# Kernel optimization log

Measured on AMD Instinct MI355X. Metric: run time of the kernel, lower is better.

The kernel has to match this reference:

```python
import jax, jax.numpy as jnp
import numpy as np

DS = 32   # self_obs_dim
DO = 32   # obstacle_obs_dim
D = DS + DO
H = 128   # obstacle_hidden_size
B = 512   # batch_size
A = 16    # num_adv_obs = 2 * num_oppo_obs


def _init_linear(key, fan_in, fan_out):
    kw, kb = jax.random.split(key)
    bound = 1.0 / np.sqrt(fan_in)
    w = jax.random.uniform(kw, (fan_in, fan_out), jnp.float32, -bound, bound)
    b = jax.random.uniform(kb, (fan_out,), jnp.float32, -bound, bound)
    return w, b


def setup_inputs() -> dict:
    key = jax.random.key(0)
    ks = jax.random.split(key, 10)
    obs = jax.random.normal(ks[0], (B, DS), jnp.float32)
    latent = jax.random.normal(ks[1], (B, A, DO), jnp.float32)
    hw1, hb1 = _init_linear(ks[2], D, H)
    hw2, hb2 = _init_linear(ks[3], H, D * H)
    vw1, vb1 = _init_linear(ks[4], H, H)
    vw2, vb2 = _init_linear(ks[5], H, H)
    aw1, ab1 = _init_linear(ks[6], 2 * H, H)
    aw2, ab2 = _init_linear(ks[7], H, H)
    aw3, ab3 = _init_linear(ks[8], H, 1)
    return {
        "obs": obs, "obs_intention_latent": latent,
        "hw1": hw1, "hb1": hb1, "hw2": hw2, "hb2": hb2,
        "vw1": vw1, "vb1": vb1, "vw2": vw2, "vb2": vb2,
        "aw1": aw1, "ab1": ab1, "aw2": aw2, "ab2": ab2,
        "aw3": aw3, "ab3": ab3,
        "num_adv_obs": A, "batch_size": B, "num_groups": 1,
    }


def reference(obs, obs_intention_latent, hw1, hb1, hw2, hb2,
              vw1, vb1, vw2, vb2, aw1, ab1, aw2, ab2, aw3, ab3,
              num_adv_obs, batch_size, num_groups):
    relu = jax.nn.relu
    # flatten opponents (batch-major, matches torch .reshape)
    obs_obstacles = obs_intention_latent.reshape(-1, DO)          # [N, DO]
    # torch .repeat(num_adv_obs, 1) tiles the batch dim
    self_rep = jnp.tile(obs[:, :DS], (num_adv_obs, 1))            # [N, DS]
    mlp_input = jnp.concatenate([self_rep, obs_obstacles], axis=1)  # [N, D]
    # hypernet: per-sample weight [N, D, H]
    h = relu(mlp_input @ hw1 + hb1)
    w = relu(h @ hw2 + hb2).reshape(-1, D, H)
    # per-sample vector-matrix product + tanh
    emb = jnp.tanh(jnp.einsum("nd,ndh->nh", mlp_input, w))        # [N, H]
    # neighbor value MLP
    vals = relu(relu(emb @ vw1 + vb1) @ vw2 + vb2)                # [N, H]
    # attention: concat with per-batch mean embedding
    emb_mean = jnp.mean(emb.reshape(batch_size, -1, H), axis=1)   # [B, H]
    mean_rep = jnp.tile(emb_mean, (num_adv_obs, 1))               # [N, H]
    att_in = jnp.concatenate([emb, mean_rep], axis=1)             # [N, 2H]
    scores = relu(relu(att_in @ aw1 + ab1) @ aw2 + ab2) @ aw3 + ab3  # [N, 1]
    att = jax.nn.softmax(scores.reshape(batch_size, -1), axis=1).reshape(-1, 1)
    weighted = (att * vals).reshape(batch_size, -1, H)
    return jnp.sum(weighted, axis=1)                              # [B, H]
```

## Files before the change

kernel.cpp:

```cpp
#include <hip/hip_runtime.h>
#include <hip/hip_bf16.h>
#include <math.h>

#define BATCH 512
#define NADV  16
#define NROWS (BATCH*NADV)
#define DS    32
#define DO    32
#define DIM   64
#define HID   128
#define WCOLS (DIM*HID)
#define LSTR  136
#define PACK_BLOCKS 276

typedef _Float16 half8 __attribute__((ext_vector_type(8)));
typedef float floatx4 __attribute__((ext_vector_type(4)));

#define XSW(c) ((((c) >> 2) & 7) << 2)

__global__ __launch_bounds__(256)
void k_prep(const float* __restrict__ obs, const float* __restrict__ latent,
            const float* __restrict__ hw1, const float* __restrict__ hb1,
            const float* __restrict__ hw2, const float* __restrict__ vw1,
            const float* __restrict__ vw2, const float* __restrict__ aw1,
            const float* __restrict__ aw2,
            _Float16* __restrict__ hf,
            _Float16* __restrict__ w2p, _Float16* __restrict__ vw1p,
            _Float16* __restrict__ vw2p, _Float16* __restrict__ aw1p,
            _Float16* __restrict__ aw2p) {
    __shared__ __align__(16) float smem[32 * 132];
    int b = blockIdx.x;
    int tid = threadIdx.x;
    if (b < PACK_BLOCKS) {
        const float* src; _Float16* dst; int N, Kt, jb, kt;
        if (b < 256)      { src = hw2; dst = w2p;  N = WCOLS; Kt = 4; jb = b >> 2; kt = b & 3; }
        else if (b < 260) { src = vw1; dst = vw1p; N = HID;   Kt = 4; jb = 0; kt = b - 256; }
        else if (b < 264) { src = vw2; dst = vw2p; N = HID;   Kt = 4; jb = 0; kt = b - 260; }
        else if (b < 272) { src = aw1; dst = aw1p; N = HID;   Kt = 8; jb = 0; kt = b - 264; }
        else              { src = aw2; dst = aw2p; N = HID;   Kt = 4; jb = 0; kt = b - 272; }
        for (int i = tid; i < 32 * 32; i += 256) {
            int r = i >> 5, c4 = (i & 31) * 4;
            *(float4*)&smem[r * 132 + c4] =
                *(const float4*)(src + (size_t)(kt * 32 + r) * N + jb * 128 + c4);
        }
        __syncthreads();
        for (int i = tid; i < 8 * 64; i += 256) {
            int ctl = i >> 6, ln = i & 63;
            int ct = jb * 8 + ctl;
            int rbase = (ln >> 4) * 8, cc = ctl * 16 + (ln & 15);
            half8 v;
#pragma unroll
            for (int e = 0; e < 8; ++e) v[e] = (_Float16)smem[(rbase + e) * 132 + cc];
            *(half8*)(dst + ((size_t)ct * Kt + kt) * 512 + ln * 8) = v;
        }
    } else {
        int n0 = (b - PACK_BLOCKS) * 16;
        int wave = tid >> 6, lane = tid & 63, l15 = lane & 15, quad = lane >> 4;
        half8 af2[2];
        {
            int n = n0 + l15;
            const float* orow = obs + (size_t)(n & (BATCH - 1)) * DS + quad * 8;
            const float* lrow = latent + (size_t)n * DO + quad * 8;
#pragma unroll
            for (int e = 0; e < 8; ++e) {
                af2[0][e] = (_Float16)orow[e];
                af2[1][e] = (_Float16)lrow[e];
            }
        }
#pragma unroll
        for (int cti = 0; cti < 2; ++cti) {
            int ct = wave * 2 + cti;
            float bb = hb1[ct * 16 + l15];
            floatx4 acc = {bb, bb, bb, bb};
#pragma unroll
            for (int ks = 0; ks < 2; ++ks) {
                const float* wsrc = hw1 + (size_t)(ks * 32 + quad * 8) * HID + ct * 16 + l15;
                half8 bf;
#pragma unroll
                for (int e = 0; e < 8; ++e) bf[e] = (_Float16)wsrc[(size_t)e * HID];
                acc = __builtin_amdgcn_mfma_f32_16x16x32_f16(af2[ks], bf, acc, 0, 0, 0);
            }
#pragma unroll
            for (int reg = 0; reg < 4; ++reg)
                hf[(size_t)(n0 + quad * 4 + reg) * HID + ct * 16 + l15] =
                    (_Float16)fmaxf(acc[reg], 0.f);
        }
    }
}

__global__ __launch_bounds__(256, 2)
void k_gemm(const _Float16* __restrict__ hf, const _Float16* __restrict__ w2p,
            const float* __restrict__ hb2, const float* __restrict__ obs,
            const float* __restrict__ latent,
            _Float16* __restrict__ embf, _Float16* __restrict__ emeanf) {
    __shared__ __align__(16) char smraw[16384 + 128];
    float (*xs_t)[64] = (float(*)[64])smraw;

    int b   = blockIdx.x;
    int tid = threadIdx.x;
    int wave = tid >> 6, lane = tid & 63, l15 = lane & 15, quad = lane >> 4;

    int jt = b & 7;
    int rt = b >> 3;
    int n0 = rt * 64;
    int j0 = jt * 16;

    for (int i = tid; i < 64 * 16; i += 256) {
        int r = i >> 4, c4 = (i & 15) * 4;
        float4 v;
        if (c4 < DS) v = *(const float4*)(obs + ((n0 + r) & (BATCH - 1)) * DS + c4);
        else         v = *(const float4*)(latent + (size_t)(n0 + r) * DO + (c4 - DS));
        xs_t[c4 + 0][r ^ XSW(c4 + 0)] = v.x;
        xs_t[c4 + 1][r ^ XSW(c4 + 1)] = v.y;
        xs_t[c4 + 2][r ^ XSW(c4 + 2)] = v.z;
        xs_t[c4 + 3][r ^ XSW(c4 + 3)] = v.w;
    }

    half8 af[4][4];
#pragma unroll
    for (int t = 0; t < 4; ++t)
#pragma unroll
        for (int ks = 0; ks < 4; ++ks)
            af[t][ks] = *(const half8*)(hf + (size_t)(n0 + t * 16 + l15) * HID
                                           + ks * 32 + quad * 8);
    __syncthreads();

    float emb_acc[4][4];
#pragma unroll
    for (int t = 0; t < 4; ++t)
#pragma unroll
        for (int reg = 0; reg < 4; ++reg) emb_acc[t][reg] = 0.f;

    const _Float16* wbase = w2p + (size_t)jt * 2048 + lane * 8;
    const _Float16* wp = wbase + (size_t)(wave * 16) * 16384;
    half8 b0 = *(const half8*)(wp + 0 * 512);
    half8 b1 = *(const half8*)(wp + 1 * 512);
    half8 b2 = *(const half8*)(wp + 2 * 512);
    half8 b3 = *(const half8*)(wp + 3 * 512);

#pragma unroll 2
    for (int i = 0; i < 16; ++i) {
        int d = wave * 16 + i;
        half8 n0_, n1_, n2_, n3_;
        if (i < 15) {
            const _Float16* np = wbase + (size_t)(d + 1) * 16384;
            n0_ = *(const half8*)(np + 0 * 512);
            n1_ = *(const half8*)(np + 1 * 512);
            n2_ = *(const half8*)(np + 2 * 512);
            n3_ = *(const half8*)(np + 3 * 512);
        }
        float bb = hb2[d * HID + j0 + l15];
        int rsw = XSW(d);
#pragma unroll
        for (int t = 0; t < 4; ++t) {
            floatx4 acc = {bb, bb, bb, bb};
            acc = __builtin_amdgcn_mfma_f32_16x16x32_f16(af[t][0], b0, acc, 0, 0, 0);
            acc = __builtin_amdgcn_mfma_f32_16x16x32_f16(af[t][1], b1, acc, 0, 0, 0);
            acc = __builtin_amdgcn_mfma_f32_16x16x32_f16(af[t][2], b2, acc, 0, 0, 0);
            acc = __builtin_amdgcn_mfma_f32_16x16x32_f16(af[t][3], b3, acc, 0, 0, 0);
            floatx4 xv = *(const floatx4*)&xs_t[d][(t * 16 + quad * 4) ^ rsw];
#pragma unroll
            for (int reg = 0; reg < 4; ++reg)
                emb_acc[t][reg] = fmaf(xv[reg], fmaxf(acc[reg], 0.f), emb_acc[t][reg]);
        }
        b0 = n0_; b1 = n1_; b2 = n2_; b3 = n3_;
    }
    __syncthreads();

    float* red = (float*)smraw;
#pragma unroll
    for (int t = 0; t < 4; ++t)
#pragma unroll
        for (int reg = 0; reg < 4; ++reg)
            red[(wave * 64 + t * 16 + quad * 4 + reg) * 16 + l15] = emb_acc[t][reg];
    __syncthreads();

    {
        float e[4];
#pragma unroll
        for (int rr = 0; rr < 4; ++rr) {
            int row = wave * 16 + quad * 4 + rr;
            float s = red[(0 * 64 + row) * 16 + l15] + red[(1 * 64 + row) * 16 + l15]
                    + red[(2 * 64 + row) * 16 + l15] + red[(3 * 64 + row) * 16 + l15];
            e[rr] = tanhf(s);
            embf[(size_t)(n0 + row) * HID + j0 + l15] = (_Float16)e[rr];
        }
        float m = e[0] + e[1] + e[2] + e[3];
        m += __shfl_xor(m, 16, 64);
        m += __shfl_xor(m, 32, 64);
        if (quad == 0)
            emeanf[(size_t)(rt * 4 + wave) * HID + j0 + l15] =
                (_Float16)(m * (1.f / 16));
    }
}

__global__ __launch_bounds__(512, 4)
void k_tail(const _Float16* __restrict__ embf, const _Float16* __restrict__ emeanf,
            const _Float16* __restrict__ vw1p, const float* __restrict__ vb1,
            const _Float16* __restrict__ vw2p, const float* __restrict__ vb2,
            const _Float16* __restrict__ aw1p, const float* __restrict__ ab1,
            const _Float16* __restrict__ aw2p, const float* __restrict__ ab2,
            const float* __restrict__ aw3, const float* __restrict__ ab3,
            float* __restrict__ out) {
    __shared__ _Float16 embs[16][LSTR];
    __shared__ _Float16 means[16][LSTR];
    __shared__ _Float16 tAs[16][LSTR];
    __shared__ _Float16 tBs[16][LSTR];
    __shared__ float scr[16][32];
    __shared__ float satt[16];
    __shared__ float att[16];
    int g = blockIdx.x;
    int n0 = g * 16;
    int tid = threadIdx.x;
    int wave = tid >> 6, lane = tid & 63, l15 = lane & 15, quad = lane >> 4;
    int ct = wave;

    {
        int m = tid >> 8, r = (tid >> 4) & 15, c8 = (tid & 15) * 8;
        if (m == 0)
            *(half8*)&embs[r][c8] = *(const half8*)(embf + (size_t)(n0 + r) * HID + c8);
        else
            *(half8*)&means[r][c8] =
                *(const half8*)(emeanf + (size_t)((n0 & 511) + r) * HID + c8);
    }
    __syncthreads();

    half8 av[4], amean[4];
#pragma unroll
    for (int ks = 0; ks < 4; ++ks) {
        av[ks]    = *(const half8*)&embs[l15][ks * 32 + quad * 8];
        amean[ks] = *(const half8*)&means[l15][ks * 32 + quad * 8];
    }

    floatx4 acc;
    {
        float bb = vb1[ct * 16 + l15];
        acc = (floatx4){bb, bb, bb, bb};
    }
#pragma unroll
    for (int ks = 0; ks < 4; ++ks) {
        half8 bfr = *(const half8*)(vw1p + ((size_t)ct * 4 + ks) * 512 + lane * 8);
        acc = __builtin_amdgcn_mfma_f32_16x16x32_f16(av[ks], bfr, acc, 0, 0, 0);
    }
#pragma unroll
    for (int reg = 0; reg < 4; ++reg)
        tAs[quad * 4 + reg][ct * 16 + l15] = (_Float16)fmaxf(acc[reg], 0.f);
    __syncthreads();

    half8 at[4];
#pragma unroll
    for (int ks = 0; ks < 4; ++ks)
        at[ks] = *(const half8*)&tAs[l15][ks * 32 + quad * 8];

    floatx4 vacc;
    {
        float bb = vb2[ct * 16 + l15];
        vacc = (floatx4){bb, bb, bb, bb};
    }
#pragma unroll
    for (int ks = 0; ks < 4; ++ks) {
        half8 bfr = *(const half8*)(vw2p + ((size_t)ct * 4 + ks) * 512 + lane * 8);
        vacc = __builtin_amdgcn_mfma_f32_16x16x32_f16(at[ks], bfr, vacc, 0, 0, 0);
    }

    floatx4 aacc;
    {
        float bb = ab1[ct * 16 + l15];
        aacc = (floatx4){bb, bb, bb, bb};
    }
#pragma unroll
    for (int ks = 0; ks < 8; ++ks) {
        half8 bfr = *(const half8*)(aw1p + ((size_t)ct * 8 + ks) * 512 + lane * 8);
        half8 a = (ks < 4) ? av[ks] : amean[ks - 4];
        aacc = __builtin_amdgcn_mfma_f32_16x16x32_f16(a, bfr, aacc, 0, 0, 0);
    }
#pragma unroll
    for (int reg = 0; reg < 4; ++reg)
        tBs[quad * 4 + reg][ct * 16 + l15] = (_Float16)fmaxf(aacc[reg], 0.f);
    __syncthreads();

    half8 aa[4];
#pragma unroll
    for (int ks = 0; ks < 4; ++ks)
        aa[ks] = *(const half8*)&tBs[l15][ks * 32 + quad * 8];

    floatx4 a2acc;
    {
        float bb = ab2[ct * 16 + l15];
        a2acc = (floatx4){bb, bb, bb, bb};
    }
#pragma unroll
    for (int ks = 0; ks < 4; ++ks) {
        half8 bfr = *(const half8*)(aw2p + ((size_t)ct * 4 + ks) * 512 + lane * 8);
        a2acc = __builtin_amdgcn_mfma_f32_16x16x32_f16(aa[ks], bfr, a2acc, 0, 0, 0);
    }
    __syncthreads();
#pragma unroll
    for (int reg = 0; reg < 4; ++reg)
        tAs[quad * 4 + reg][ct * 16 + l15] = (_Float16)fmaxf(a2acc[reg], 0.f);
    __syncthreads();

    {
        int r = tid >> 5, ch = tid & 31;
        float p = 0.f;
#pragma unroll
        for (int k = 0; k < 4; ++k)
            p += (float)tAs[r][ch * 4 + k] * aw3[ch * 4 + k];
        scr[r][ch] = p;
    }
    __syncthreads();
    if (tid < 16) {
        float s = ab3[0];
#pragma unroll
        for (int ch = 0; ch < 32; ++ch) s += scr[tid][ch];
        satt[tid] = s;
    }
    __syncthreads();
    if (tid < 16) {
        float m = -1e30f;
#pragma unroll
        for (int a = 0; a < 16; ++a) m = fmaxf(m, satt[a]);
        float S = 0.f;
#pragma unroll
        for (int a = 0; a < 16; ++a) S += expf(satt[a] - m);
        att[tid] = expf(satt[tid] - m) / S;
    }
    __syncthreads();

    {
        float p = 0.f;
#pragma unroll
        for (int reg = 0; reg < 4; ++reg)
            p += att[quad * 4 + reg] * fmaxf(vacc[reg], 0.f);
        p += __shfl_xor(p, 16, 64);
        p += __shfl_xor(p, 32, 64);
        if (quad == 0) out[(size_t)g * HID + ct * 16 + l15] = p;
    }
}

extern "C" void kernel_launch(void* const* d_in, const int* in_sizes, int n_in,
                              void* d_out, int out_size, void* d_ws, size_t ws_size,
                              hipStream_t stream) {
    const float* obs = (const float*)d_in[0];
    const float* lat = (const float*)d_in[1];
    const float* hw1 = (const float*)d_in[2];
    const float* hb1 = (const float*)d_in[3];
    const float* hw2 = (const float*)d_in[4];
    const float* hb2 = (const float*)d_in[5];
    const float* vw1 = (const float*)d_in[6];
    const float* vb1 = (const float*)d_in[7];
    const float* vw2 = (const float*)d_in[8];
    const float* vb2 = (const float*)d_in[9];
    const float* aw1 = (const float*)d_in[10];
    const float* ab1 = (const float*)d_in[11];
    const float* aw2 = (const float*)d_in[12];
    const float* ab2 = (const float*)d_in[13];
    const float* aw3 = (const float*)d_in[14];
    const float* ab3 = (const float*)d_in[15];
    float* out = (float*)d_out;

    char* ws = (char*)d_ws;
    _Float16*  hf     = (_Float16*)ws;  ws += (size_t)NROWS * HID * 2;
    _Float16*  w2p    = (_Float16*)ws;  ws += (size_t)WCOLS * HID * 2;
    _Float16*  embf   = (_Float16*)ws;  ws += (size_t)NROWS * HID * 2;
    _Float16*  emeanf = (_Float16*)ws;  ws += (size_t)BATCH * HID * 2;
    _Float16*  vw1p   = (_Float16*)ws;  ws += (size_t)HID * HID * 2;
    _Float16*  vw2p   = (_Float16*)ws;  ws += (size_t)HID * HID * 2;
    _Float16*  aw1p   = (_Float16*)ws;  ws += (size_t)2 * HID * HID * 2;
    _Float16*  aw2p   = (_Float16*)ws;  ws += (size_t)HID * HID * 2;

    hipLaunchKernelGGL(k_prep, dim3(PACK_BLOCKS + NROWS / 16), dim3(256), 0, stream,
                       obs, lat, hw1, hb1, hw2, vw1, vw2, aw1, aw2,
                       hf, w2p, vw1p, vw2p, aw1p, aw2p);
    hipLaunchKernelGGL(k_gemm, dim3(1024), dim3(256), 0, stream,
                       hf, w2p, hb2, obs, lat, embf, emeanf);
    hipLaunchKernelGGL(k_tail, dim3(BATCH), dim3(512), 0, stream,
                       embf, emeanf, vw1p, vb1, vw2p, vb2,
                       aw1p, ab1, aw2p, ab2, aw3, ab3, out);
}
```

Baseline: 134.5 us.

## Stream hypernet weight tiles into LDS with async double-buffered global_load_lds

The main hypernet GEMM kernel now stages each wave's weight tiles into a per-wave double-buffered LDS region using global_load_lds, prefetching two d-steps ahead with explicit vmcnt waits. Before, it used register prefetch of the next step. The bias slice is also preloaded into shared memory instead of being read from global memory on every iteration. The aim is to hide global-load latency better and lower register pressure so occupancy can go to 3 blocks per CU. In exchange, LDS use grows to about 52KB per block, and correctness depends on hand-placed waitcnt counts and scheduling barriers.

Result: no change. 132.6 us (-1.4%).

```diff
diff --git a/kernel.cpp b/kernel.cpp
--- a/kernel.cpp
+++ b/kernel.cpp
@@ -15,6 +15,12 @@
 
 typedef _Float16 half8 __attribute__((ext_vector_type(8)));
 typedef float floatx4 __attribute__((ext_vector_type(4)));
+
+__device__ inline void async_ld16(void* lds, const void* g) {
+    __builtin_amdgcn_global_load_lds(
+        (const __attribute__((address_space(1))) void*)g,
+        (__attribute__((address_space(3))) void*)lds, 16, 0, 0);
+}
 
 #define XSW(c) ((((c) >> 2) & 7) << 2)
 
@@ -88,13 +94,15 @@
     }
 }
 
-__global__ __launch_bounds__(256, 2)
-void k_gemm(const _Float16* __restrict__ hf, const _Float16* __restrict__ w2p,
-            const float* __restrict__ hb2, const float* __restrict__ obs,
-            const float* __restrict__ latent,
-            _Float16* __restrict__ embf, _Float16* __restrict__ emeanf) {
-    __shared__ __align__(16) char smraw[16384 + 128];
-    float (*xs_t)[64] = (float(*)[64])smraw;
+__global__ __launch_bounds__(256, 3)
+void k_hyper(const _Float16* __restrict__ hf, const _Float16* __restrict__ w2p,
+             const float* __restrict__ hb2, const float* __restrict__ obs,
+             const float* __restrict__ latent,
+             _Float16* __restrict__ embf, _Float16* __restrict__ emeanf) {
+    __shared__ __align__(16) char smraw[53248];
+    _Float16 (*Bs)[2][2048] = (_Float16(*)[2][2048])smraw;
+    float (*xs_t)[64] = (float(*)[64])(smraw + 32768);
+    float* bias_s = (float*)(smraw + 49152);
 
     int b   = blockIdx.x;
     int tid = threadIdx.x;
@@ -115,6 +123,8 @@
         xs_t[c4 + 2][r ^ XSW(c4 + 2)] = v.z;
         xs_t[c4 + 3][r ^ XSW(c4 + 3)] = v.w;
     }
+    for (int i = tid; i < 64 * 16; i += 256)
+        bias_s[i] = hb2[(i >> 4) * HID + j0 + (i & 15)];
 
     half8 af[4][4];
 #pragma unroll
@@ -123,6 +133,15 @@
         for (int ks = 0; ks < 4; ++ks)
             af[t][ks] = *(const half8*)(hf + (size_t)(n0 + t * 16 + l15) * HID
                                            + ks * 32 + quad * 8);
+
+    const _Float16* wbase = w2p + (size_t)jt * 2048 + lane * 8;
+#pragma unroll
+    for (int p = 0; p < 2; ++p) {
+        const _Float16* src = wbase + (size_t)(wave * 16 + p) * 16384;
+#pragma unroll
+        for (int kt = 0; kt < 4; ++kt)
+            async_ld16(&Bs[wave][p][kt * 512], src + kt * 512);
+    }
     __syncthreads();
 
     float emb_acc[4][4];
@@ -131,25 +150,19 @@
 #pragma unroll
         for (int reg = 0; reg < 4; ++reg) emb_acc[t][reg] = 0.f;
 
-    const _Float16* wbase = w2p + (size_t)jt * 2048 + lane * 8;
-    const _Float16* wp = wbase + (size_t)(wave * 16) * 16384;
-    half8 b0 = *(const half8*)(wp + 0 * 512);
-    half8 b1 = *(const half8*)(wp + 1 * 512);
-    half8 b2 = *(const half8*)(wp + 2 * 512);
-    half8 b3 = *(const half8*)(wp + 3 * 512);
-
-#pragma unroll 2
+#pragma unroll
     for (int i = 0; i < 16; ++i) {
+        if (i < 15) asm volatile("s_waitcnt vmcnt(4)" ::: "memory");
+        else        asm volatile("s_waitcnt vmcnt(0)" ::: "memory");
+        __builtin_amdgcn_sched_barrier(0);
+
         int d = wave * 16 + i;
-        half8 n0_, n1_, n2_, n3_;
-        if (i < 15) {
-            const _Float16* np = wbase + (size_t)(d + 1) * 16384;
-            n0_ = *(const half8*)(np + 0 * 512);
-            n1_ = *(const half8*)(np + 1 * 512);
-            n2_ = *(const half8*)(np + 2 * 512);
-            n3_ = *(const half8*)(np + 3 * 512);
-        }
-        float bb = hb2[d * HID + j0 + l15];
+        int buf = i & 1;
+        half8 b0 = *(const half8*)&Bs[wave][buf][0 * 512 + lane * 8];
+        half8 b1 = *(const half8*)&Bs[wave][buf][1 * 512 + lane * 8];
+        half8 b2 = *(const half8*)&Bs[wave][buf][2 * 512 + lane * 8];
+        half8 b3 = *(const half8*)&Bs[wave][buf][3 * 512 + lane * 8];
+        float bb = bias_s[d * 16 + l15];
         int rsw = XSW(d);
 #pragma unroll
         for (int t = 0; t < 4; ++t) {
@@ -163,11 +176,17 @@
             for (int reg = 0; reg < 4; ++reg)
                 emb_acc[t][reg] = fmaf(xv[reg], fmaxf(acc[reg], 0.f), emb_acc[t][reg]);
         }
-        b0 = n0_; b1 = n1_; b2 = n2_; b3 = n3_;
-    }
-    __syncthreads();
-
-    float* red = (float*)smraw;
+        __builtin_amdgcn_sched_barrier(0);
+        if (i + 2 < 16) {
+            const _Float16* src = wbase + (size_t)(d + 2) * 16384;
+#pragma unroll
+            for (int kt = 0; kt < 4; ++kt)
+                async_ld16(&Bs[wave][buf][kt * 512], src + kt * 512);
+        }
+    }
+    __syncthreads();
+
+    float* red = (float*)(smraw + 32768);
 #pragma unroll
     for (int t = 0; t < 4; ++t)
 #pragma unroll
@@ -372,7 +391,7 @@
     hipLaunchKernelGGL(k_prep, dim3(PACK_BLOCKS + NROWS / 16), dim3(256), 0, stream,
                        obs, lat, hw1, hb1, hw2, vw1, vw2, aw1, aw2,
                        hf, w2p, vw1p, vw2p, aw1p, aw2p);
-    hipLaunchKernelGGL(k_gemm, dim3(1024), dim3(256), 0, stream,
+    hipLaunchKernelGGL(k_hyper, dim3(1024), dim3(256), 0, stream,
                        hf, w2p, hb2, obs, lat, embf, emeanf);
     hipLaunchKernelGGL(k_tail, dim3(BATCH), dim3(512), 0, stream,
                        embf, emeanf, vw1p, vb1, vw2p, vb2,
```
